# Kernel tuning notes

Hardware: AMD Instinct MI355X
Metric: run time of the kernel (lower is better)

## Reference

```python
import jax, jax.numpy as jnp
import numpy as np

B, H, W, DIM = 8, 64, 64, 256
HEADS, DH = 8, 64
HID = HEADS * DH  # 512
EPS = 1e-5


def setup_inputs() -> dict:
    key = jax.random.key(0)
    k0, k1, k2 = jax.random.split(key, 3)
    return {
        "x": jax.random.normal(k0, (B, H, W, DIM), dtype=jnp.float32),
        "w_qkv": jax.random.normal(k1, (DIM, 3 * HID), dtype=jnp.float32) / np.sqrt(DIM),
        "gn_scale": jnp.ones((HID,), jnp.float32),
        "gn_bias": jnp.zeros((HID,), jnp.float32),
        "w_out": jax.random.normal(k2, (HID, DIM), dtype=jnp.float32) / np.sqrt(HID),
        "b_out": jnp.zeros((DIM,), jnp.float32),
    }


def reference(x, w_qkv, gn_scale, gn_bias, w_out, b_out):
    b, h, w, c = x.shape
    n = h * w
    scale = DH ** -0.5
    # 1x1 conv (no bias) == channel matmul
    qkv = jnp.einsum('bxyc,cf->bxyf', x, w_qkv)
    q, k, v = jnp.split(qkv, 3, axis=-1)
    # 'b x y (h c) -> b h c (x y)'
    to_heads = lambda t: t.reshape(b, n, HEADS, DH).transpose(0, 2, 3, 1)
    q, k, v = map(to_heads, (q, k, v))  # [b, heads, d, n]
    q = jax.nn.softmax(q, axis=-2) * scale  # softmax over feature dim d
    k = jax.nn.softmax(k, axis=-1)          # softmax over token dim n
    context = jnp.einsum('bhdn,bhen->bhde', k, v)   # small d x e context
    out = jnp.einsum('bhde,bhdn->bhen', context, q)  # [b, heads, e, n]
    # 'b h c (x y) -> b x y (h c)'
    out = out.transpose(0, 3, 1, 2).reshape(b, h, w, HID)
    # GroupNorm with 1 group: normalize over (H, W, C) per sample
    mu = out.mean(axis=(1, 2, 3), keepdims=True)
    var = out.var(axis=(1, 2, 3), keepdims=True)
    out = (out - mu) * jax.lax.rsqrt(var + EPS) * gn_scale + gn_bias
    # final 1x1 conv with bias
    return jnp.einsum('bxyf,fc->bxyc', out, w_out) + b_out
```

## Files before the change

kernel.cpp:

```cpp
#include <hip/hip_runtime.h>


typedef unsigned short ushort_t;
typedef __attribute__((ext_vector_type(8))) short short8;
typedef __attribute__((ext_vector_type(4))) float floatx4;

__device__ __forceinline__ float b2f(ushort_t u) {
  unsigned int i = ((unsigned int)u) << 16;
  float f;
  __builtin_memcpy(&f, &i, 4);
  return f;
}
__device__ __forceinline__ ushort_t f2b(float f) {
  unsigned int i;
  __builtin_memcpy(&i, &f, 4);
  unsigned int r = (i + 0x7FFFu + ((i >> 16) & 1u)) >> 16;
  return (ushort_t)r;
}

__device__ __forceinline__ void load_lds16(const ushort_t* g, ushort_t* l) {
  __builtin_amdgcn_global_load_lds(
      (const __attribute__((address_space(1))) unsigned int*)g,
      (__attribute__((address_space(3))) unsigned int*)l, 16, 0, 0);
}

__global__ __launch_bounds__(256) void cast_f32_bf16(
    const float* __restrict__ in, ushort_t* __restrict__ out) {
  long i = ((long)blockIdx.x * 256 + threadIdx.x) * 4;
  float4 v = *(const float4*)(in + i);
  ushort4 o;
  o.x = f2b(v.x);
  o.y = f2b(v.y);
  o.z = f2b(v.z);
  o.w = f2b(v.w);
  *(ushort4*)(out + i) = o;
}

__global__ __launch_bounds__(256) void transpose_f32_bf16(
    const float* __restrict__ in, ushort_t* __restrict__ out, int R, int C,
    const float* __restrict__ scale) {
  __shared__ ushort_t t[32][33];
  int c0 = blockIdx.x * 32, r0 = blockIdx.y * 32;
  int tx = threadIdx.x & 31, ty = threadIdx.x >> 5;
  for (int i = 0; i < 32; i += 8) {
    float s = scale ? scale[r0 + ty + i] : 1.0f;
    t[ty + i][tx] = f2b(in[(long)(r0 + ty + i) * C + c0 + tx] * s);
  }
  __syncthreads();
  for (int i = 0; i < 32; i += 8)
    out[(long)(c0 + ty + i) * R + r0 + tx] = t[tx][ty + i];
}

__global__ __launch_bounds__(64) void prep_gw_kernel(
    const float* __restrict__ gn_scale, const float* __restrict__ gn_bias,
    const float* __restrict__ w_out, const float* __restrict__ b_out,
    float* __restrict__ gw1, float* __restrict__ bias2) {
  int c = blockIdx.x * 64 + threadIdx.x;
  float g1 = 0.f, b2 = 0.f;
  for (int f = 0; f < 512; ++f) {
    float w = w_out[f * 256 + c];
    g1 += gn_scale[f] * w;
    b2 += gn_bias[f] * w;
  }
  gw1[c] = g1;
  bias2[c] = b2 + b_out[c];
}

template <int MODE, bool SWAP>
__global__ __launch_bounds__(256) void gemm_tpl(
    const ushort_t* __restrict__ A, const ushort_t* __restrict__ Bt,
    void* __restrict__ Cv, int M, int K, int F,
    const float* __restrict__ murs, const float* __restrict__ gw1,
    const float* __restrict__ bias2) {
  __shared__ __align__(16) ushort_t As[128][32];
  __shared__ __align__(16) ushort_t Bs[128][32];
  int tid = threadIdx.x;
  long m0 = (long)(SWAP ? blockIdx.y : blockIdx.x) * 128;
  long f0 = (long)(SWAP ? blockIdx.x : blockIdx.y) * 128;
  int wv = tid >> 6, lane = tid & 63;
  int wm = wv & 1, wf = wv >> 1;
  int l15 = lane & 15, quad = lane >> 4;

  floatx4 acc[4][4];
  floatx4 zero = {0.f, 0.f, 0.f, 0.f};
  for (int i = 0; i < 4; i++)
    for (int j = 0; j < 4; j++) acc[i][j] = zero;

  for (int k0 = 0; k0 < K; k0 += 32) {
    __syncthreads();
#pragma unroll
    for (int r = 0; r < 2; ++r) {
      int chunk = r * 256 + tid;
      int row = chunk >> 2;
      int kc = chunk & 3;
      load_lds16(A + (m0 + row) * (long)K + k0 + kc * 8, &As[row][kc * 8]);
      load_lds16(Bt + (f0 + row) * (long)K + k0 + kc * 8, &Bs[row][kc * 8]);
    }
    __syncthreads();
    short8 af[4], bfr[4];
#pragma unroll
    for (int mt = 0; mt < 4; mt++)
      af[mt] = *(const short8*)(&As[wm * 64 + mt * 16 + l15][quad * 8]);
#pragma unroll
    for (int ft = 0; ft < 4; ft++)
      bfr[ft] = *(const short8*)(&Bs[wf * 64 + ft * 16 + l15][quad * 8]);
#pragma unroll
    for (int mt = 0; mt < 4; mt++)
#pragma unroll
      for (int ft = 0; ft < 4; ft++)
        acc[mt][ft] = __builtin_amdgcn_mfma_f32_16x16x32_bf16(
            af[mt], bfr[ft], acc[mt][ft], 0, 0, 0);
  }

  {
    float* C = (float*)Cv;
    int b = (int)(m0 >> 12);
    float mu = murs[b * 2], rs = murs[b * 2 + 1];
#pragma unroll
    for (int mt = 0; mt < 4; mt++)
#pragma unroll
      for (int ft = 0; ft < 4; ft++) {
        long col = f0 + wf * 64 + ft * 16 + l15;
        float c1 = bias2[col] - rs * mu * gw1[col];
#pragma unroll
        for (int r = 0; r < 4; r++) {
          long row = m0 + wm * 64 + mt * 16 + quad * 4 + r;
          C[row * F + col] = rs * acc[mt][ft][r] + c1;
        }
      }
  }
}

__global__ __launch_bounds__(256) void kvctx_kernel(
    const ushort_t* __restrict__ xb, const ushort_t* __restrict__ wqkvT,
    float* __restrict__ ctxP, float* __restrict__ ksumP) {
  __shared__ __align__(16) char lds[32768];
  ushort_t* As = (ushort_t*)lds;
  ushort_t* Bs = (ushort_t*)(lds + 16384);
  ushort_t* kTs = (ushort_t*)lds;
  ushort_t* vTs = (ushort_t*)(lds + 16384);

  int bh = blockIdx.x, cy = blockIdx.y;
  int b = bh >> 3, h = bh & 7;
  int tid = threadIdx.x, wv = tid >> 6, lane = tid & 63;
  int wm = wv & 1, wfk = wv >> 1;
  int l15 = lane & 15, quad = lane >> 4;
  long m0 = (long)b * 4096 + cy * 128;

  floatx4 acc[4][4];
  floatx4 zero = {0.f, 0.f, 0.f, 0.f};
  for (int i = 0; i < 4; i++)
    for (int j = 0; j < 4; j++) acc[i][j] = zero;

  for (int k0 = 0; k0 < 256; k0 += 64) {
    __syncthreads();
#pragma unroll
    for (int r = 0; r < 4; ++r) {
      int chunk = r * 256 + tid;
      int row = chunk >> 3;
      int kc = chunk & 7;
      int gc = kc ^ (row & 7);
      long arow = (row < 64 ? 512 : 960) + h * 64 + row;
      load_lds16(wqkvT + arow * 256 + k0 + gc * 8, As + chunk * 8);
      load_lds16(xb + (m0 + row) * 256 + k0 + gc * 8, Bs + chunk * 8);
    }
    __syncthreads();
#pragma unroll
    for (int ks = 0; ks < 2; ++ks) {
      short8 af[4], bfr[4];
#pragma unroll
      for (int mt = 0; mt < 4; mt++) {
        int row = wfk * 64 + mt * 16 + l15;
        int slot = (ks * 4 + quad) ^ (row & 7);
        af[mt] = *(const short8*)(As + row * 64 + slot * 8);
      }
#pragma unroll
      for (int ft = 0; ft < 4; ft++) {
        int rowb = wm * 64 + ft * 16 + l15;
        int slot = (ks * 4 + quad) ^ (rowb & 7);
        bfr[ft] = *(const short8*)(Bs + rowb * 64 + slot * 8);
      }
#pragma unroll
      for (int mt = 0; mt < 4; mt++)
#pragma unroll
        for (int ft = 0; ft < 4; ft++)
          acc[mt][ft] = __builtin_amdgcn_mfma_f32_16x16x32_bf16(
              af[mt], bfr[ft], acc[mt][ft], 0, 0, 0);
    }
  }
  __syncthreads();

  {
    ushort_t* T = wfk ? vTs : kTs;
#pragma unroll
    for (int mt = 0; mt < 4; mt++)
#pragma unroll
      for (int ft = 0; ft < 4; ft++) {
        int n = wm * 64 + ft * 16 + l15;
        int c = n >> 3, u = n & 7;
#pragma unroll
        for (int r = 0; r < 4; r++) {
          int d = mt * 16 + quad * 4 + r;
          float v = acc[mt][ft][r];
          if (!wfk) v = __expf(v);
          int slot = (c & 8) | ((c ^ d) & 7);
          T[d * 128 + slot * 8 + u] = f2b(v);
        }
      }
  }
  __syncthreads();

  floatx4 cacc[4], acc1;
  for (int i = 0; i < 4; i++) cacc[i] = zero;
  acc1 = zero;
  short8 ones;
#pragma unroll
  for (int u = 0; u < 8; ++u) ones[u] = (short)0x3F80;
#pragma unroll
  for (int ks = 0; ks < 4; ++ks) {
    int d = wv * 16 + l15;
    int cidx = ks * 4 + quad;
    int sa = (cidx & 8) | ((cidx ^ d) & 7);
    short8 a = *(const short8*)(kTs + d * 128 + sa * 8);
    short8 bf[4];
#pragma unroll
    for (int ft = 0; ft < 4; ++ft) {
      int e = ft * 16 + l15;
      int sb = (cidx & 8) | ((cidx ^ e) & 7);
      bf[ft] = *(const short8*)(vTs + e * 128 + sb * 8);
    }
#pragma unroll
    for (int ft = 0; ft < 4; ++ft)
      cacc[ft] = __builtin_amdgcn_mfma_f32_16x16x32_bf16(a, bf[ft], cacc[ft],
                                                         0, 0, 0);
    acc1 = __builtin_amdgcn_mfma_f32_16x16x32_bf16(a, ones, acc1, 0, 0, 0);
  }
  float* cb = ctxP + ((long)cy * 64 + bh) * 4096;
#pragma unroll
  for (int ft = 0; ft < 4; ++ft)
    *(floatx4*)&cb[(ft * 16 + l15) * 64 + wv * 16 + quad * 4] = cacc[ft];
  if (l15 == 0) {
    float* kb = ksumP + ((long)cy * 64 + bh) * 64;
    *(floatx4*)&kb[wv * 16 + quad * 4] = acc1;
  }
}

__global__ __launch_bounds__(256) void reduce_kernel(
    const float* __restrict__ ctxP, const float* __restrict__ ksumP,
    ushort_t* __restrict__ ctxB) {
  int bid = blockIdx.x;
  int bh = bid >> 4;
  int j = (bid & 15) * 256 + threadIdx.x;
  int e = j >> 6, d = j & 63;
  float ks = 0.f;
#pragma unroll
  for (int c = 0; c < 32; ++c) ks += ksumP[((long)c * 64 + bh) * 64 + d];
  float s = 0.f;
#pragma unroll
  for (int c = 0; c < 32; ++c) s += ctxP[((long)c * 64 + bh) * 4096 + j];
  int slot = (d >> 3) ^ (e & 7);
  ctxB[(long)bh * 4096 + e * 64 + slot * 8 + (d & 7)] = f2b(s / ks);
}

__global__ __launch_bounds__(256, 4) void qattn_kernel(
    const ushort_t* __restrict__ xb, const ushort_t* __restrict__ wqT,
    const ushort_t* __restrict__ ctxB, ushort_t* __restrict__ A2,
    float* __restrict__ gstats) {
  __shared__ __align__(16) char lds[32800];
  ushort_t* As = (ushort_t*)lds;
  ushort_t* Bs = (ushort_t*)(lds + 16384);
  ushort_t* P = (ushort_t*)lds;
  float* red = (float*)(lds + 32768);

  int tid = threadIdx.x;
  int bx = blockIdx.x, by = blockIdx.y;
  long m0 = (long)bx * 128;
  long f0 = (long)by * 128;
  int wv = tid >> 6, lane = tid & 63;
  int wm = wv & 1, wf = wv >> 1;
  int l15 = lane & 15, quad = lane >> 4;
  int b = bx >> 5;

  floatx4 acc[4][4];
  floatx4 zero = {0.f, 0.f, 0.f, 0.f};
  for (int i = 0; i < 4; i++)
    for (int j = 0; j < 4; j++) acc[i][j] = zero;

  for (int k0 = 0; k0 < 256; k0 += 64) {
    __syncthreads();
#pragma unroll
    for (int r = 0; r < 4; ++r) {
      int chunk = r * 256 + tid;
      int row = chunk >> 3;
      int kc = chunk & 7;
      int gc = kc ^ (row & 7);
      load_lds16(xb + (m0 + row) * 256 + k0 + gc * 8, As + chunk * 8);
      load_lds16(wqT + (f0 + row) * 256 + k0 + gc * 8, Bs + chunk * 8);
    }
    __syncthreads();
#pragma unroll
    for (int ks = 0; ks < 2; ++ks) {
      short8 af[4], bfr[4];
#pragma unroll
      for (int mt = 0; mt < 4; mt++) {
        int row = wm * 64 + mt * 16 + l15;
        int slot = (ks * 4 + quad) ^ (row & 7);
        af[mt] = *(const short8*)(As + row * 64 + slot * 8);
      }
#pragma unroll
      for (int ft = 0; ft < 4; ft++) {
        int rowb = wf * 64 + ft * 16 + l15;
        int slot = (ks * 4 + quad) ^ (rowb & 7);
        bfr[ft] = *(const short8*)(Bs + rowb * 64 + slot * 8);
      }
#pragma unroll
      for (int mt = 0; mt < 4; mt++)
#pragma unroll
        for (int ft = 0; ft < 4; ft++)
          acc[mt][ft] = __builtin_amdgcn_mfma_f32_16x16x32_bf16(
              af[mt], bfr[ft], acc[mt][ft], 0, 0, 0);
    }
  }

  const ushort_t* cg = ctxB + ((long)(b * 8 + by * 2 + wf)) * 4096;
  short8 cfr0[4];
#pragma unroll
  for (int ft = 0; ft < 4; ++ft) {
    int e = ft * 16 + l15;
    int slot = quad ^ (e & 7);
    cfr0[ft] = *(const short8*)(cg + e * 64 + slot * 8);
  }

  __syncthreads();

  float rs[4][4];
#pragma unroll
  for (int mt = 0; mt < 4; mt++)
#pragma unroll
    for (int r = 0; r < 4; r++) rs[mt][r] = 0.f;
#pragma unroll
  for (int mt = 0; mt < 4; mt++)
#pragma unroll
    for (int ft = 0; ft < 4; ft++)
#pragma unroll
      for (int r = 0; r < 4; r++) {
        float e = __expf(acc[mt][ft][r]);
        acc[mt][ft][r] = e;
        rs[mt][r] += e;
      }
#pragma unroll
  for (int mt = 0; mt < 4; mt++)
#pragma unroll
    for (int r = 0; r < 4; r++) {
      float t = rs[mt][r];
      t += __shfl_xor(t, 1);
      t += __shfl_xor(t, 2);
      t += __shfl_xor(t, 4);
      t += __shfl_xor(t, 8);
      rs[mt][r] = 0.125f / t;
    }

  {
    ushort_t* Pw = P + wf * 8192;
#pragma unroll
    for (int mt = 0; mt < 4; mt++)
#pragma unroll
      for (int ft = 0; ft < 4; ft++) {
        int d = ft * 16 + l15;
#pragma unroll
        for (int r = 0; r < 4; r++) {
          int row = wm * 64 + mt * 16 + quad * 4 + r;
          int slot = (d >> 3) ^ (row & 7);
          Pw[row * 64 + slot * 8 + (d & 7)] = f2b(acc[mt][ft][r] * rs[mt][r]);
        }
      }
  }

  short8 cfr1[4];
#pragma unroll
  for (int ft = 0; ft < 4; ++ft) {
    int e = ft * 16 + l15;
    int slot = (4 + quad) ^ (e & 7);
    cfr1[ft] = *(const short8*)(cg + e * 64 + slot * 8);
  }

  floatx4 o[4][4];
  for (int i = 0; i < 4; i++)
    for (int j = 0; j < 4; j++) o[i][j] = zero;
  {
    const ushort_t* Pr = P + wf * 8192;
    short8 af[4];
#pragma unroll
    for (int mt = 0; mt < 4; mt++) {
      int row = wm * 64 + mt * 16 + l15;
      int slot = quad ^ (row & 7);
      af[mt] = *(const short8*)(Pr + row * 64 + slot * 8);
    }
#pragma unroll
    for (int mt = 0; mt < 4; mt++)
#pragma unroll
      for (int ft = 0; ft < 4; ft++)
        o[mt][ft] = __builtin_amdgcn_mfma_f32_16x16x32_bf16(af[mt], cfr0[ft],
                                                            o[mt][ft], 0, 0,
                                                            0);
#pragma unroll
    for (int mt = 0; mt < 4; mt++) {
      int row = wm * 64 + mt * 16 + l15;
      int slot = (4 + quad) ^ (row & 7);
      af[mt] = *(const short8*)(Pr + row * 64 + slot * 8);
    }
#pragma unroll
    for (int mt = 0; mt < 4; mt++)
#pragma unroll
      for (int ft = 0; ft < 4; ft++)
        o[mt][ft] = __builtin_amdgcn_mfma_f32_16x16x32_bf16(af[mt], cfr1[ft],
                                                            o[mt][ft], 0, 0,
                                                            0);
  }

  float lsum = 0.f, lss = 0.f;
#pragma unroll
  for (int mt = 0; mt < 4; mt++)
#pragma unroll
    for (int ft = 0; ft < 4; ft++) {
      long col = f0 + wf * 64 + ft * 16 + l15;
#pragma unroll
      for (int r = 0; r < 4; r++) {
        long row = m0 + wm * 64 + mt * 16 + quad * 4 + r;
        float v = o[mt][ft][r];
        A2[row * 512 + col] = f2b(v);
        lsum += v;
        lss += v * v;
      }
    }
  for (int s = 32; s > 0; s >>= 1) {
    lsum += __shfl_xor(lsum, s);
    lss += __shfl_xor(lss, s);
  }
  if (lane == 0) {
    red[wv * 2] = lsum;
    red[wv * 2 + 1] = lss;
  }
  __syncthreads();
  if (tid == 0) {
    float a = 0.f, c = 0.f;
    for (int w2 = 0; w2 < 4; w2++) {
      a += red[w2 * 2];
      c += red[w2 * 2 + 1];
    }
    atomicAdd(&gstats[b * 2], a);
    atomicAdd(&gstats[b * 2 + 1], c);
  }
}

__global__ __launch_bounds__(64) void finalize_murs(
    const float* __restrict__ gstats, float* __restrict__ murs) {
  int tid = threadIdx.x;
  if (tid < 8) {
    float cnt = 4096.f * 512.f;
    float mu = gstats[tid * 2] / cnt;
    float var = gstats[tid * 2 + 1] / cnt - mu * mu;
    murs[tid * 2] = mu;
    murs[tid * 2 + 1] = rsqrtf(var + 1e-5f);
  }
}

extern "C" void kernel_launch(void* const* d_in, const int* in_sizes, int n_in,
                              void* d_out, int out_size, void* d_ws,
                              size_t ws_size, hipStream_t stream) {
  const float* x = (const float*)d_in[0];
  const float* w_qkv = (const float*)d_in[1];
  const float* gn_scale = (const float*)d_in[2];
  const float* gn_bias = (const float*)d_in[3];
  const float* w_out = (const float*)d_in[4];
  const float* b_out = (const float*)d_in[5];
  float* out = (float*)d_out;

  char* w = (char*)d_ws;
  ushort_t* xb = (ushort_t*)(w + 0);
  ushort_t* A2 = (ushort_t*)(w + 16777216);
  float* ctxP = (float*)(w + 50331648);
  float* ksumP = (float*)(w + 83886080);
  ushort_t* wqkvT = (ushort_t*)(w + 84410368);
  ushort_t* w2T = (ushort_t*)(w + 85196800);
  ushort_t* ctxB = (ushort_t*)(w + 85458944);
  float* gstats = (float*)(w + 85983232);
  float* murs = (float*)(w + 85983296);
  float* bias2 = (float*)(w + 85983360);
  float* gw1 = (float*)(w + 85984384);

  hipMemsetAsync(gstats, 0, 64, stream);

  cast_f32_bf16<<<8388608 / 4 / 256, 256, 0, stream>>>(x, xb);
  transpose_f32_bf16<<<dim3(1536 / 32, 256 / 32), 256, 0, stream>>>(
      w_qkv, wqkvT, 256, 1536, nullptr);
  transpose_f32_bf16<<<dim3(256 / 32, 512 / 32), 256, 0, stream>>>(
      w_out, w2T, 512, 256, gn_scale);
  prep_gw_kernel<<<4, 64, 0, stream>>>(gn_scale, gn_bias, w_out, b_out, gw1,
                                       bias2);
  kvctx_kernel<<<dim3(64, 32), 256, 0, stream>>>(xb, wqkvT, ctxP, ksumP);
  reduce_kernel<<<1024, 256, 0, stream>>>(ctxP, ksumP, ctxB);
  qattn_kernel<<<dim3(256, 4), 256, 0, stream>>>(xb, wqkvT, ctxB, A2, gstats);
  finalize_murs<<<1, 64, 0, stream>>>(gstats, murs);
  gemm_tpl<2, false><<<dim3(256, 2), 256, 0, stream>>>(
      A2, w2T, out, 32768, 512, 256, murs, gw1, bias2);
}
```

Measured before the change: 230.4 us.

## Widen qattn tiles to full Q width and loop kvctx over sub-chunks

kvctx now loops over four 128-token sub-chunks per block and accumulates context in registers, so the grid is four times smaller. That cuts partial-context writes and the reduce kernel's summation from 32 partials to 8. qattn now uses 512-thread blocks that each compute all 512 Q features for a 128-row tile, so each x tile is loaded once instead of four times. Output is staged through a 64KB LDS buffer for coalesced 16-byte stores to A2. The cost is a large LDS footprint (about 128KB per block) and 64 accumulator floatx4 per thread, which limits occupancy to one or two blocks per CU and raises register pressure.

```diff
diff --git a/kernel.cpp b/kernel.cpp
--- a/kernel.cpp
+++ b/kernel.cpp
@@ -145,96 +145,100 @@
   int tid = threadIdx.x, wv = tid >> 6, lane = tid & 63;
   int wm = wv & 1, wfk = wv >> 1;
   int l15 = lane & 15, quad = lane >> 4;
-  long m0 = (long)b * 4096 + cy * 128;
-
-  floatx4 acc[4][4];
+
   floatx4 zero = {0.f, 0.f, 0.f, 0.f};
-  for (int i = 0; i < 4; i++)
-    for (int j = 0; j < 4; j++) acc[i][j] = zero;
-
-  for (int k0 = 0; k0 < 256; k0 += 64) {
-    __syncthreads();
-#pragma unroll
-    for (int r = 0; r < 4; ++r) {
-      int chunk = r * 256 + tid;
-      int row = chunk >> 3;
-      int kc = chunk & 7;
-      int gc = kc ^ (row & 7);
-      long arow = (row < 64 ? 512 : 960) + h * 64 + row;
-      load_lds16(wqkvT + arow * 256 + k0 + gc * 8, As + chunk * 8);
-      load_lds16(xb + (m0 + row) * 256 + k0 + gc * 8, Bs + chunk * 8);
-    }
-    __syncthreads();
-#pragma unroll
-    for (int ks = 0; ks < 2; ++ks) {
-      short8 af[4], bfr[4];
-#pragma unroll
-      for (int mt = 0; mt < 4; mt++) {
-        int row = wfk * 64 + mt * 16 + l15;
-        int slot = (ks * 4 + quad) ^ (row & 7);
-        af[mt] = *(const short8*)(As + row * 64 + slot * 8);
-      }
-#pragma unroll
-      for (int ft = 0; ft < 4; ft++) {
-        int rowb = wm * 64 + ft * 16 + l15;
-        int slot = (ks * 4 + quad) ^ (rowb & 7);
-        bfr[ft] = *(const short8*)(Bs + rowb * 64 + slot * 8);
-      }
-#pragma unroll
-      for (int mt = 0; mt < 4; mt++)
-#pragma unroll
-        for (int ft = 0; ft < 4; ft++)
-          acc[mt][ft] = __builtin_amdgcn_mfma_f32_16x16x32_bf16(
-              af[mt], bfr[ft], acc[mt][ft], 0, 0, 0);
-    }
-  }
-  __syncthreads();
-
-  {
-    ushort_t* T = wfk ? vTs : kTs;
-#pragma unroll
-    for (int mt = 0; mt < 4; mt++)
-#pragma unroll
-      for (int ft = 0; ft < 4; ft++) {
-        int n = wm * 64 + ft * 16 + l15;
-        int c = n >> 3, u = n & 7;
-#pragma unroll
-        for (int r = 0; r < 4; r++) {
-          int d = mt * 16 + quad * 4 + r;
-          float v = acc[mt][ft][r];
-          if (!wfk) v = __expf(v);
-          int slot = (c & 8) | ((c ^ d) & 7);
-          T[d * 128 + slot * 8 + u] = f2b(v);
-        }
-      }
-  }
-  __syncthreads();
-
   floatx4 cacc[4], acc1;
   for (int i = 0; i < 4; i++) cacc[i] = zero;
   acc1 = zero;
   short8 ones;
 #pragma unroll
   for (int u = 0; u < 8; ++u) ones[u] = (short)0x3F80;
-#pragma unroll
-  for (int ks = 0; ks < 4; ++ks) {
-    int d = wv * 16 + l15;
-    int cidx = ks * 4 + quad;
-    int sa = (cidx & 8) | ((cidx ^ d) & 7);
-    short8 a = *(const short8*)(kTs + d * 128 + sa * 8);
-    short8 bf[4];
-#pragma unroll
-    for (int ft = 0; ft < 4; ++ft) {
-      int e = ft * 16 + l15;
-      int sb = (cidx & 8) | ((cidx ^ e) & 7);
-      bf[ft] = *(const short8*)(vTs + e * 128 + sb * 8);
-    }
-#pragma unroll
-    for (int ft = 0; ft < 4; ++ft)
-      cacc[ft] = __builtin_amdgcn_mfma_f32_16x16x32_bf16(a, bf[ft], cacc[ft],
-                                                         0, 0, 0);
-    acc1 = __builtin_amdgcn_mfma_f32_16x16x32_bf16(a, ones, acc1, 0, 0, 0);
-  }
+
+  for (int sub = 0; sub < 4; ++sub) {
+    long m0 = (long)b * 4096 + cy * 512 + sub * 128;
+    floatx4 acc[4][4];
+    for (int i = 0; i < 4; i++)
+      for (int j = 0; j < 4; j++) acc[i][j] = zero;
+
+    for (int k0 = 0; k0 < 256; k0 += 64) {
+      __syncthreads();
+#pragma unroll
+      for (int r = 0; r < 4; ++r) {
+        int chunk = r * 256 + tid;
+        int row = chunk >> 3;
+        int kc = chunk & 7;
+        int gc = kc ^ (row & 7);
+        long arow = (row < 64 ? 512 : 960) + h * 64 + row;
+        load_lds16(wqkvT + arow * 256 + k0 + gc * 8, As + chunk * 8);
+        load_lds16(xb + (m0 + row) * 256 + k0 + gc * 8, Bs + chunk * 8);
+      }
+      __syncthreads();
+#pragma unroll
+      for (int ks = 0; ks < 2; ++ks) {
+        short8 af[4], bfr[4];
+#pragma unroll
+        for (int mt = 0; mt < 4; mt++) {
+          int row = wfk * 64 + mt * 16 + l15;
+          int slot = (ks * 4 + quad) ^ (row & 7);
+          af[mt] = *(const short8*)(As + row * 64 + slot * 8);
+        }
+#pragma unroll
+        for (int ft = 0; ft < 4; ft++) {
+          int rowb = wm * 64 + ft * 16 + l15;
+          int slot = (ks * 4 + quad) ^ (rowb & 7);
+          bfr[ft] = *(const short8*)(Bs + rowb * 64 + slot * 8);
+        }
+#pragma unroll
+        for (int mt = 0; mt < 4; mt++)
+#pragma unroll
+          for (int ft = 0; ft < 4; ft++)
+            acc[mt][ft] = __builtin_amdgcn_mfma_f32_16x16x32_bf16(
+                af[mt], bfr[ft], acc[mt][ft], 0, 0, 0);
+      }
+    }
+    __syncthreads();
+
+    {
+      ushort_t* T = wfk ? vTs : kTs;
+#pragma unroll
+      for (int mt = 0; mt < 4; mt++)
+#pragma unroll
+        for (int ft = 0; ft < 4; ft++) {
+          int n = wm * 64 + ft * 16 + l15;
+          int c = n >> 3, u = n & 7;
+#pragma unroll
+          for (int r = 0; r < 4; r++) {
+            int d = mt * 16 + quad * 4 + r;
+            float v = acc[mt][ft][r];
+            if (!wfk) v = __expf(v);
+            int slot = (c & 8) | ((c ^ d) & 7);
+            T[d * 128 + slot * 8 + u] = f2b(v);
+          }
+        }
+    }
+    __syncthreads();
+
+#pragma unroll
+    for (int ks = 0; ks < 4; ++ks) {
+      int d = wv * 16 + l15;
+      int cidx = ks * 4 + quad;
+      int sa = (cidx & 8) | ((cidx ^ d) & 7);
+      short8 a = *(const short8*)(kTs + d * 128 + sa * 8);
+      short8 bf[4];
+#pragma unroll
+      for (int ft = 0; ft < 4; ++ft) {
+        int e = ft * 16 + l15;
+        int sb = (cidx & 8) | ((cidx ^ e) & 7);
+        bf[ft] = *(const short8*)(vTs + e * 128 + sb * 8);
+      }
+#pragma unroll
+      for (int ft = 0; ft < 4; ++ft)
+        cacc[ft] = __builtin_amdgcn_mfma_f32_16x16x32_bf16(a, bf[ft], cacc[ft],
+                                                           0, 0, 0);
+      acc1 = __builtin_amdgcn_mfma_f32_16x16x32_bf16(a, ones, acc1, 0, 0, 0);
+    }
+  }
+
   float* cb = ctxP + ((long)cy * 64 + bh) * 4096;
 #pragma unroll
   for (int ft = 0; ft < 4; ++ft)
@@ -254,53 +258,60 @@
   int e = j >> 6, d = j & 63;
   float ks = 0.f;
 #pragma unroll
-  for (int c = 0; c < 32; ++c) ks += ksumP[((long)c * 64 + bh) * 64 + d];
+  for (int c = 0; c < 8; ++c) ks += ksumP[((long)c * 64 + bh) * 64 + d];
   float s = 0.f;
 #pragma unroll
-  for (int c = 0; c < 32; ++c) s += ctxP[((long)c * 64 + bh) * 4096 + j];
+  for (int c = 0; c < 8; ++c) s += ctxP[((long)c * 64 + bh) * 4096 + j];
   int slot = (d >> 3) ^ (e & 7);
   ctxB[(long)bh * 4096 + e * 64 + slot * 8 + (d & 7)] = f2b(s / ks);
 }
 
-__global__ __launch_bounds__(256, 4) void qattn_kernel(
+__global__ __launch_bounds__(512, 2) void qattn_kernel(
     const ushort_t* __restrict__ xb, const ushort_t* __restrict__ wqT,
     const ushort_t* __restrict__ ctxB, ushort_t* __restrict__ A2,
     float* __restrict__ gstats) {
-  __shared__ __align__(16) char lds[32800];
+  __shared__ __align__(16) char lds[131136];
   ushort_t* As = (ushort_t*)lds;
   ushort_t* Bs = (ushort_t*)(lds + 16384);
   ushort_t* P = (ushort_t*)lds;
-  float* red = (float*)(lds + 32768);
+  ushort_t* O = (ushort_t*)(lds + 65536);
+  float* red = (float*)(lds + 131072);
 
   int tid = threadIdx.x;
-  int bx = blockIdx.x, by = blockIdx.y;
+  int bx = blockIdx.x;
   long m0 = (long)bx * 128;
-  long f0 = (long)by * 128;
   int wv = tid >> 6, lane = tid & 63;
-  int wm = wv & 1, wf = wv >> 1;
+  int wm = wv >> 2, wf = wv & 3;
   int l15 = lane & 15, quad = lane >> 4;
   int b = bx >> 5;
 
-  floatx4 acc[4][4];
   floatx4 zero = {0.f, 0.f, 0.f, 0.f};
+  floatx4 acc[4][8];
   for (int i = 0; i < 4; i++)
-    for (int j = 0; j < 4; j++) acc[i][j] = zero;
+    for (int j = 0; j < 8; j++) acc[i][j] = zero;
 
   for (int k0 = 0; k0 < 256; k0 += 64) {
     __syncthreads();
 #pragma unroll
-    for (int r = 0; r < 4; ++r) {
-      int chunk = r * 256 + tid;
+    for (int r = 0; r < 2; ++r) {
+      int chunk = r * 512 + tid;
       int row = chunk >> 3;
       int kc = chunk & 7;
       int gc = kc ^ (row & 7);
       load_lds16(xb + (m0 + row) * 256 + k0 + gc * 8, As + chunk * 8);
-      load_lds16(wqT + (f0 + row) * 256 + k0 + gc * 8, Bs + chunk * 8);
+    }
+#pragma unroll
+    for (int r = 0; r < 8; ++r) {
+      int chunk = r * 512 + tid;
+      int row = chunk >> 3;
+      int kc = chunk & 7;
+      int gc = kc ^ (row & 7);
+      load_lds16(wqT + row * 256 + k0 + gc * 8, Bs + chunk * 8);
     }
     __syncthreads();
 #pragma unroll
     for (int ks = 0; ks < 2; ++ks) {
-      short8 af[4], bfr[4];
+      short8 af[4], bfr[8];
 #pragma unroll
       for (int mt = 0; mt < 4; mt++) {
         int row = wm * 64 + mt * 16 + l15;
@@ -308,131 +319,133 @@
         af[mt] = *(const short8*)(As + row * 64 + slot * 8);
       }
 #pragma unroll
-      for (int ft = 0; ft < 4; ft++) {
-        int rowb = wf * 64 + ft * 16 + l15;
+      for (int ft = 0; ft < 8; ft++) {
+        int rowb = wf * 128 + ft * 16 + l15;
         int slot = (ks * 4 + quad) ^ (rowb & 7);
         bfr[ft] = *(const short8*)(Bs + rowb * 64 + slot * 8);
       }
 #pragma unroll
       for (int mt = 0; mt < 4; mt++)
 #pragma unroll
-        for (int ft = 0; ft < 4; ft++)
+        for (int ft = 0; ft < 8; ft++)
           acc[mt][ft] = __builtin_amdgcn_mfma_f32_16x16x32_bf16(
               af[mt], bfr[ft], acc[mt][ft], 0, 0, 0);
     }
   }
-
-  const ushort_t* cg = ctxB + ((long)(b * 8 + by * 2 + wf)) * 4096;
-  short8 cfr0[4];
-#pragma unroll
-  for (int ft = 0; ft < 4; ++ft) {
-    int e = ft * 16 + l15;
-    int slot = quad ^ (e & 7);
-    cfr0[ft] = *(const short8*)(cg + e * 64 + slot * 8);
-  }
-
   __syncthreads();
 
-  float rs[4][4];
+  float rs[2][4][4];
+#pragma unroll
+  for (int hh = 0; hh < 2; hh++)
+#pragma unroll
+    for (int mt = 0; mt < 4; mt++)
+#pragma unroll
+      for (int r = 0; r < 4; r++) rs[hh][mt][r] = 0.f;
 #pragma unroll
   for (int mt = 0; mt < 4; mt++)
 #pragma unroll
-    for (int r = 0; r < 4; r++) rs[mt][r] = 0.f;
-#pragma unroll
-  for (int mt = 0; mt < 4; mt++)
-#pragma unroll
-    for (int ft = 0; ft < 4; ft++)
+    for (int ft = 0; ft < 8; ft++)
 #pragma unroll
       for (int r = 0; r < 4; r++) {
         float e = __expf(acc[mt][ft][r]);
         acc[mt][ft][r] = e;
-        rs[mt][r] += e;
-      }
+        rs[ft >> 2][mt][r] += e;
+      }
+#pragma unroll
+  for (int hh = 0; hh < 2; hh++)
+#pragma unroll
+    for (int mt = 0; mt < 4; mt++)
+#pragma unroll
+      for (int r = 0; r < 4; r++) {
+        float t = rs[hh][mt][r];
+        t += __shfl_xor(t, 1);
+        t += __shfl_xor(t, 2);
+        t += __shfl_xor(t, 4);
+        t += __shfl_xor(t, 8);
+        rs[hh][mt][r] = 0.125f / t;
+      }
+
+  floatx4 o[4][8];
+  for (int i = 0; i < 4; i++)
+    for (int j = 0; j < 8; j++) o[i][j] = zero;
+  ushort_t* Pw = P + wv * 4096;
+#pragma unroll
+  for (int hh = 0; hh < 2; ++hh) {
+#pragma unroll
+    for (int mt = 0; mt < 4; mt++)
+#pragma unroll
+      for (int ftl = 0; ftl < 4; ftl++) {
+        int d = ftl * 16 + l15;
+#pragma unroll
+        for (int r = 0; r < 4; r++) {
+          int rl = mt * 16 + quad * 4 + r;
+          int slot = (d >> 3) ^ (rl & 7);
+          Pw[rl * 64 + slot * 8 + (d & 7)] =
+              f2b(acc[mt][hh * 4 + ftl][r] * rs[hh][mt][r]);
+        }
+      }
+    const ushort_t* cg = ctxB + ((long)(b * 8 + wf * 2 + hh)) * 4096;
+#pragma unroll
+    for (int ks2 = 0; ks2 < 2; ++ks2) {
+      short8 af2[4], cfr[4];
+#pragma unroll
+      for (int mt = 0; mt < 4; mt++) {
+        int rl = mt * 16 + l15;
+        int slot = (ks2 * 4 + quad) ^ (rl & 7);
+        af2[mt] = *(const short8*)(Pw + rl * 64 + slot * 8);
+      }
+#pragma unroll
+      for (int fe = 0; fe < 4; fe++) {
+        int e = fe * 16 + l15;
+        int slot = (ks2 * 4 + quad) ^ (e & 7);
+        cfr[fe] = *(const short8*)(cg + e * 64 + slot * 8);
+      }
+#pragma unroll
+      for (int mt = 0; mt < 4; mt++)
+#pragma unroll
+        for (int fe = 0; fe < 4; fe++)
+          o[mt][hh * 4 + fe] = __builtin_amdgcn_mfma_f32_16x16x32_bf16(
+              af2[mt], cfr[fe], o[mt][hh * 4 + fe], 0, 0, 0);
+    }
+  }
+
+  float lsum = 0.f, lss = 0.f;
 #pragma unroll
   for (int mt = 0; mt < 4; mt++)
 #pragma unroll
-    for (int r = 0; r < 4; r++) {
-      float t = rs[mt][r];
-      t += __shfl_xor(t, 1);
-      t += __shfl_xor(t, 2);
-      t += __shfl_xor(t, 4);
-      t += __shfl_xor(t, 8);
-      rs[mt][r] = 0.125f / t;
-    }
-
-  {
-    ushort_t* Pw = P + wf * 8192;
-#pragma unroll
-    for (int mt = 0; mt < 4; mt++)
-#pragma unroll
-      for (int ft = 0; ft < 4; ft++) {
-        int d = ft * 16 + l15;
-#pragma unroll
-        for (int r = 0; r < 4; r++) {
-          int row = wm * 64 + mt * 16 + quad * 4 + r;
-          int slot = (d >> 3) ^ (row & 7);
-          Pw[row * 64 + slot * 8 + (d & 7)] = f2b(acc[mt][ft][r] * rs[mt][r]);
-        }
-      }
-  }
-
-  short8 cfr1[4];
-#pragma unroll
-  for (int ft = 0; ft < 4; ++ft) {
-    int e = ft * 16 + l15;
-    int slot = (4 + quad) ^ (e & 7);
-    cfr1[ft] = *(const short8*)(cg + e * 64 + slot * 8);
-  }
-
-  floatx4 o[4][4];
-  for (int i = 0; i < 4; i++)
-    for (int j = 0; j < 4; j++) o[i][j] = zero;
-  {
-    const ushort_t* Pr = P + wf * 8192;
-    short8 af[4];
-#pragma unroll
-    for (int mt = 0; mt < 4; mt++) {
-      int row = wm * 64 + mt * 16 + l15;
-      int slot = quad ^ (row & 7);
-      af[mt] = *(const short8*)(Pr + row * 64 + slot * 8);
-    }
-#pragma unroll
-    for (int mt = 0; mt < 4; mt++)
-#pragma unroll
-      for (int ft = 0; ft < 4; ft++)
-        o[mt][ft] = __builtin_amdgcn_mfma_f32_16x16x32_bf16(af[mt], cfr0[ft],
-                                                            o[mt][ft], 0, 0,
-                                                            0);
-#pragma unroll
-    for (int mt = 0; mt < 4; mt++) {
-      int row = wm * 64 + mt * 16 + l15;
-      int slot = (4 + quad) ^ (row & 7);
-      af[mt] = *(const short8*)(Pr + row * 64 + slot * 8);
-    }
-#pragma unroll
-    for (int mt = 0; mt < 4; mt++)
-#pragma unroll
-      for (int ft = 0; ft < 4; ft++)
-        o[mt][ft] = __builtin_amdgcn_mfma_f32_16x16x32_bf16(af[mt], cfr1[ft],
-                                                            o[mt][ft], 0, 0,
-                                                            0);
-  }
-
-  float lsum = 0.f, lss = 0.f;
-#pragma unroll
-  for (int mt = 0; mt < 4; mt++)
-#pragma unroll
-    for (int ft = 0; ft < 4; ft++) {
-      long col = f0 + wf * 64 + ft * 16 + l15;
+    for (int ft = 0; ft < 8; ft++)
 #pragma unroll
       for (int r = 0; r < 4; r++) {
-        long row = m0 + wm * 64 + mt * 16 + quad * 4 + r;
         float v = o[mt][ft][r];
-        A2[row * 512 + col] = f2b(v);
         lsum += v;
         lss += v * v;
       }
-    }
+
+#pragma unroll
+  for (int wmp = 0; wmp < 2; ++wmp) {
+    if (wm == wmp) {
+#pragma unroll
+      for (int mt = 0; mt < 4; mt++)
+#pragma unroll
+        for (int ft = 0; ft < 8; ft++) {
+          int col = wf * 128 + ft * 16 + l15;
+#pragma unroll
+          for (int r = 0; r < 4; r++) {
+            int rl = mt * 16 + quad * 4 + r;
+            O[rl * 512 + col] = f2b(o[mt][ft][r]);
+          }
+        }
+    }
+    __syncthreads();
+    ushort_t* a2g = A2 + (m0 + wmp * 64) * 512;
+#pragma unroll
+    for (int s = 0; s < 8; ++s) {
+      int off = s * 4096 + tid * 8;
+      *(short8*)(a2g + off) = *(const short8*)(O + off);
+    }
+    __syncthreads();
+  }
+
   for (int s = 32; s > 0; s >>= 1) {
     lsum += __shfl_xor(lsum, s);
     lss += __shfl_xor(lss, s);
@@ -444,7 +457,7 @@
   __syncthreads();
   if (tid == 0) {
     float a = 0.f, c = 0.f;
-    for (int w2 = 0; w2 < 4; w2++) {
+    for (int w2 = 0; w2 < 8; w2++) {
       a += red[w2 * 2];
       c += red[w2 * 2 + 1];
     }
@@ -498,9 +511,9 @@
       w_out, w2T, 512, 256, gn_scale);
   prep_gw_kernel<<<4, 64, 0, stream>>>(gn_scale, gn_bias, w_out, b_out, gw1,
                                        bias2);
-  kvctx_kernel<<<dim3(64, 32), 256, 0, stream>>>(xb, wqkvT, ctxP, ksumP);
+  kvctx_kernel<<<dim3(64, 8), 256, 0, stream>>>(xb, wqkvT, ctxP, ksumP);
   reduce_kernel<<<1024, 256, 0, stream>>>(ctxP, ksumP, ctxB);
-  qattn_kernel<<<dim3(256, 4), 256, 0, stream>>>(xb, wqkvT, ctxB, A2, gstats);
+  qattn_kernel<<<256, 512, 0, stream>>>(xb, wqkvT, ctxB, A2, gstats);
   finalize_murs<<<1, 64, 0, stream>>>(gstats, murs);
   gemm_tpl<2, false><<<dim3(256, 2), 256, 0, stream>>>(
       A2, w2T, out, 32768, 512, 256, murs, gw1, bias2);
```

After: 221.7 us. 3.8% less time.

## Accumulate kv context over 4 token chunks per block; stage qattn output via LDS

Applied to the files above, without the earlier changes.

kvctx now loops over four 128-token sub-chunks inside each block and keeps the context accumulators in registers. This cuts the grid from 32 to 8 partial slices per head and shrinks the partial-context write and reduce traffic by 4x. qattn now stages its bf16 output tile through swizzled LDS so it can be written to A2 as coalesced 16-byte row stores, replacing scattered 2-byte stores. The trade-off is fewer kvctx blocks (512), so less parallelism, plus extra barriers and LDS traffic in qattn.

```diff
diff --git a/kernel.cpp b/kernel.cpp
--- a/kernel.cpp
+++ b/kernel.cpp
@@ -145,96 +145,100 @@
   int tid = threadIdx.x, wv = tid >> 6, lane = tid & 63;
   int wm = wv & 1, wfk = wv >> 1;
   int l15 = lane & 15, quad = lane >> 4;
-  long m0 = (long)b * 4096 + cy * 128;
-
-  floatx4 acc[4][4];
+
   floatx4 zero = {0.f, 0.f, 0.f, 0.f};
-  for (int i = 0; i < 4; i++)
-    for (int j = 0; j < 4; j++) acc[i][j] = zero;
-
-  for (int k0 = 0; k0 < 256; k0 += 64) {
-    __syncthreads();
-#pragma unroll
-    for (int r = 0; r < 4; ++r) {
-      int chunk = r * 256 + tid;
-      int row = chunk >> 3;
-      int kc = chunk & 7;
-      int gc = kc ^ (row & 7);
-      long arow = (row < 64 ? 512 : 960) + h * 64 + row;
-      load_lds16(wqkvT + arow * 256 + k0 + gc * 8, As + chunk * 8);
-      load_lds16(xb + (m0 + row) * 256 + k0 + gc * 8, Bs + chunk * 8);
-    }
-    __syncthreads();
-#pragma unroll
-    for (int ks = 0; ks < 2; ++ks) {
-      short8 af[4], bfr[4];
-#pragma unroll
-      for (int mt = 0; mt < 4; mt++) {
-        int row = wfk * 64 + mt * 16 + l15;
-        int slot = (ks * 4 + quad) ^ (row & 7);
-        af[mt] = *(const short8*)(As + row * 64 + slot * 8);
-      }
-#pragma unroll
-      for (int ft = 0; ft < 4; ft++) {
-        int rowb = wm * 64 + ft * 16 + l15;
-        int slot = (ks * 4 + quad) ^ (rowb & 7);
-        bfr[ft] = *(const short8*)(Bs + rowb * 64 + slot * 8);
-      }
-#pragma unroll
-      for (int mt = 0; mt < 4; mt++)
-#pragma unroll
-        for (int ft = 0; ft < 4; ft++)
-          acc[mt][ft] = __builtin_amdgcn_mfma_f32_16x16x32_bf16(
-              af[mt], bfr[ft], acc[mt][ft], 0, 0, 0);
-    }
-  }
-  __syncthreads();
-
-  {
-    ushort_t* T = wfk ? vTs : kTs;
-#pragma unroll
-    for (int mt = 0; mt < 4; mt++)
-#pragma unroll
-      for (int ft = 0; ft < 4; ft++) {
-        int n = wm * 64 + ft * 16 + l15;
-        int c = n >> 3, u = n & 7;
-#pragma unroll
-        for (int r = 0; r < 4; r++) {
-          int d = mt * 16 + quad * 4 + r;
-          float v = acc[mt][ft][r];
-          if (!wfk) v = __expf(v);
-          int slot = (c & 8) | ((c ^ d) & 7);
-          T[d * 128 + slot * 8 + u] = f2b(v);
-        }
-      }
-  }
-  __syncthreads();
-
   floatx4 cacc[4], acc1;
   for (int i = 0; i < 4; i++) cacc[i] = zero;
   acc1 = zero;
   short8 ones;
 #pragma unroll
   for (int u = 0; u < 8; ++u) ones[u] = (short)0x3F80;
-#pragma unroll
-  for (int ks = 0; ks < 4; ++ks) {
-    int d = wv * 16 + l15;
-    int cidx = ks * 4 + quad;
-    int sa = (cidx & 8) | ((cidx ^ d) & 7);
-    short8 a = *(const short8*)(kTs + d * 128 + sa * 8);
-    short8 bf[4];
-#pragma unroll
-    for (int ft = 0; ft < 4; ++ft) {
-      int e = ft * 16 + l15;
-      int sb = (cidx & 8) | ((cidx ^ e) & 7);
-      bf[ft] = *(const short8*)(vTs + e * 128 + sb * 8);
-    }
-#pragma unroll
-    for (int ft = 0; ft < 4; ++ft)
-      cacc[ft] = __builtin_amdgcn_mfma_f32_16x16x32_bf16(a, bf[ft], cacc[ft],
-                                                         0, 0, 0);
-    acc1 = __builtin_amdgcn_mfma_f32_16x16x32_bf16(a, ones, acc1, 0, 0, 0);
-  }
+
+  for (int sub = 0; sub < 4; ++sub) {
+    long m0 = (long)b * 4096 + cy * 512 + sub * 128;
+    floatx4 acc[4][4];
+    for (int i = 0; i < 4; i++)
+      for (int j = 0; j < 4; j++) acc[i][j] = zero;
+
+    for (int k0 = 0; k0 < 256; k0 += 64) {
+      __syncthreads();
+#pragma unroll
+      for (int r = 0; r < 4; ++r) {
+        int chunk = r * 256 + tid;
+        int row = chunk >> 3;
+        int kc = chunk & 7;
+        int gc = kc ^ (row & 7);
+        long arow = (row < 64 ? 512 : 960) + h * 64 + row;
+        load_lds16(wqkvT + arow * 256 + k0 + gc * 8, As + chunk * 8);
+        load_lds16(xb + (m0 + row) * 256 + k0 + gc * 8, Bs + chunk * 8);
+      }
+      __syncthreads();
+#pragma unroll
+      for (int ks = 0; ks < 2; ++ks) {
+        short8 af[4], bfr[4];
+#pragma unroll
+        for (int mt = 0; mt < 4; mt++) {
+          int row = wfk * 64 + mt * 16 + l15;
+          int slot = (ks * 4 + quad) ^ (row & 7);
+          af[mt] = *(const short8*)(As + row * 64 + slot * 8);
+        }
+#pragma unroll
+        for (int ft = 0; ft < 4; ft++) {
+          int rowb = wm * 64 + ft * 16 + l15;
+          int slot = (ks * 4 + quad) ^ (rowb & 7);
+          bfr[ft] = *(const short8*)(Bs + rowb * 64 + slot * 8);
+        }
+#pragma unroll
+        for (int mt = 0; mt < 4; mt++)
+#pragma unroll
+          for (int ft = 0; ft < 4; ft++)
+            acc[mt][ft] = __builtin_amdgcn_mfma_f32_16x16x32_bf16(
+                af[mt], bfr[ft], acc[mt][ft], 0, 0, 0);
+      }
+    }
+    __syncthreads();
+
+    {
+      ushort_t* T = wfk ? vTs : kTs;
+#pragma unroll
+      for (int mt = 0; mt < 4; mt++)
+#pragma unroll
+        for (int ft = 0; ft < 4; ft++) {
+          int n = wm * 64 + ft * 16 + l15;
+          int c = n >> 3, u = n & 7;
+#pragma unroll
+          for (int r = 0; r < 4; r++) {
+            int d = mt * 16 + quad * 4 + r;
+            float v = acc[mt][ft][r];
+            if (!wfk) v = __expf(v);
+            int slot = (c & 8) | ((c ^ d) & 7);
+            T[d * 128 + slot * 8 + u] = f2b(v);
+          }
+        }
+    }
+    __syncthreads();
+
+#pragma unroll
+    for (int ks = 0; ks < 4; ++ks) {
+      int d = wv * 16 + l15;
+      int cidx = ks * 4 + quad;
+      int sa = (cidx & 8) | ((cidx ^ d) & 7);
+      short8 a = *(const short8*)(kTs + d * 128 + sa * 8);
+      short8 bf[4];
+#pragma unroll
+      for (int ft = 0; ft < 4; ++ft) {
+        int e = ft * 16 + l15;
+        int sb = (cidx & 8) | ((cidx ^ e) & 7);
+        bf[ft] = *(const short8*)(vTs + e * 128 + sb * 8);
+      }
+#pragma unroll
+      for (int ft = 0; ft < 4; ++ft)
+        cacc[ft] = __builtin_amdgcn_mfma_f32_16x16x32_bf16(a, bf[ft], cacc[ft],
+                                                           0, 0, 0);
+      acc1 = __builtin_amdgcn_mfma_f32_16x16x32_bf16(a, ones, acc1, 0, 0, 0);
+    }
+  }
+
   float* cb = ctxP + ((long)cy * 64 + bh) * 4096;
 #pragma unroll
   for (int ft = 0; ft < 4; ++ft)
@@ -254,10 +258,10 @@
   int e = j >> 6, d = j & 63;
   float ks = 0.f;
 #pragma unroll
-  for (int c = 0; c < 32; ++c) ks += ksumP[((long)c * 64 + bh) * 64 + d];
+  for (int c = 0; c < 8; ++c) ks += ksumP[((long)c * 64 + bh) * 64 + d];
   float s = 0.f;
 #pragma unroll
-  for (int c = 0; c < 32; ++c) s += ctxP[((long)c * 64 + bh) * 4096 + j];
+  for (int c = 0; c < 8; ++c) s += ctxP[((long)c * 64 + bh) * 4096 + j];
   int slot = (d >> 3) ^ (e & 7);
   ctxB[(long)bh * 4096 + e * 64 + slot * 8 + (d & 7)] = f2b(s / ks);
 }
@@ -270,6 +274,7 @@
   ushort_t* As = (ushort_t*)lds;
   ushort_t* Bs = (ushort_t*)(lds + 16384);
   ushort_t* P = (ushort_t*)lds;
+  ushort_t* Od = (ushort_t*)lds;
   float* red = (float*)(lds + 32768);
 
   int tid = threadIdx.x;
@@ -422,17 +427,44 @@
 #pragma unroll
   for (int mt = 0; mt < 4; mt++)
 #pragma unroll
-    for (int ft = 0; ft < 4; ft++) {
-      long col = f0 + wf * 64 + ft * 16 + l15;
+    for (int ft = 0; ft < 4; ft++)
 #pragma unroll
       for (int r = 0; r < 4; r++) {
-        long row = m0 + wm * 64 + mt * 16 + quad * 4 + r;
         float v = o[mt][ft][r];
-        A2[row * 512 + col] = f2b(v);
         lsum += v;
         lss += v * v;
       }
-    }
+
+  __syncthreads();
+
+#pragma unroll
+  for (int mt = 0; mt < 4; mt++)
+#pragma unroll
+    for (int ft = 0; ft < 4; ft++) {
+      int cl = wf * 64 + ft * 16 + l15;
+      int c = cl >> 3, u = cl & 7;
+#pragma unroll
+      for (int r = 0; r < 4; r++) {
+        int rl = wm * 64 + mt * 16 + quad * 4 + r;
+        int slot = (c & 8) | ((c ^ rl) & 7);
+        Od[rl * 128 + slot * 8 + u] = f2b(o[mt][ft][r]);
+      }
+    }
+  __syncthreads();
+
+  {
+    ushort_t* a2g = A2 + m0 * 512 + f0;
+#pragma unroll
+    for (int s = 0; s < 8; ++s) {
+      int off = s * 2048 + tid * 8;
+      int row = off >> 7;
+      int c2 = (off & 127) >> 3;
+      int slot = (c2 & 8) | ((c2 ^ row) & 7);
+      *(short8*)(a2g + (long)row * 512 + c2 * 8) =
+          *(const short8*)(Od + row * 128 + slot * 8);
+    }
+  }
+
   for (int s = 32; s > 0; s >>= 1) {
     lsum += __shfl_xor(lsum, s);
     lss += __shfl_xor(lss, s);
@@ -498,7 +530,7 @@
       w_out, w2T, 512, 256, gn_scale);
   prep_gw_kernel<<<4, 64, 0, stream>>>(gn_scale, gn_bias, w_out, b_out, gw1,
                                        bias2);
-  kvctx_kernel<<<dim3(64, 32), 256, 0, stream>>>(xb, wqkvT, ctxP, ksumP);
+  kvctx_kernel<<<dim3(64, 8), 256, 0, stream>>>(xb, wqkvT, ctxP, ksumP);
   reduce_kernel<<<1024, 256, 0, stream>>>(ctxP, ksumP, ctxB);
   qattn_kernel<<<dim3(256, 4), 256, 0, stream>>>(xb, wqkvT, ctxB, A2, gstats);
   finalize_murs<<<1, 64, 0, stream>>>(gstats, murs);
```

Result: slower. 236.7 us (+2.7%).
